# Optimization experiments

Hardware: AMD Instinct MI355X
Metric: run time of the kernel (lower is better)

## Reference

```python
import jax, jax.numpy as jnp
import numpy as np

H, IN, L, R = 128, 64, 3, 7
Nc, Na, Nx = 10000, 40000, 100000
NS = (Nc, Na, Nx)
ES = (50000, 100000, 100000, 150000, 200000, 200000, 200000)
# relation order: cc, c->a, a->c, aa, a->x, x->a, xx  (0=core,1=agg,2=access)
SRC_T = (0, 0, 1, 1, 1, 2, 2)
DST_T = (0, 1, 0, 1, 2, 1, 2)


def setup_inputs() -> dict:
    key = jax.random.key(0)
    ks = iter(jax.random.split(key, 80))
    d = {}
    for name, n in (("x_core", Nc), ("x_agg", Na), ("x_access", Nx)):
        d[name] = jax.random.normal(next(ks), (n, IN), jnp.float32)
    for r in range(R):
        d[f"src{r}"] = jax.random.randint(next(ks), (ES[r],), 0, NS[SRC_T[r]])
        d[f"dst{r}"] = jax.random.randint(next(ks), (ES[r],), 0, NS[DST_T[r]])
        d[f"ea{r}"] = jax.random.normal(next(ks), (ES[r], 3), jnp.float32)

    def w(k, shape, fan):
        return (jax.random.normal(k, shape, jnp.float32) / np.float32(np.sqrt(fan)))

    for nt in ("core", "agg", "access"):
        d[f"linW_{nt}"] = w(next(ks), (IN, H), IN)
        d[f"linb_{nt}"] = jnp.zeros((H,), jnp.float32)
    d["eW"] = w(next(ks), (L, R, 3, H), 3)       # GINEConv edge Linear(3->H)
    d["eb"] = jnp.zeros((L, R, H), jnp.float32)
    d["W1"] = w(next(ks), (L, R, H, H), H)        # MLP first Linear
    d["b1"] = jnp.zeros((L, R, H), jnp.float32)
    d["g1"] = jnp.ones((L, R, H), jnp.float32)    # BatchNorm gamma
    d["be1"] = jnp.zeros((L, R, H), jnp.float32)  # BatchNorm beta
    d["W2"] = w(next(ks), (L, R, H, H), H)        # MLP second Linear
    d["b2"] = jnp.zeros((L, R, H), jnp.float32)
    return d


def _forward(x_core, x_agg, x_access,
             linW_core, linb_core, linW_agg, linb_agg, linW_access, linb_access,
             eW, eb, W1, b1, g1, be1, W2, b2, srcs, dsts, eas):
    elu = jax.nn.elu
    h = [elu(x_core @ linW_core + linb_core),
         elu(x_agg @ linW_agg + linb_agg),
         elu(x_access @ linW_access + linb_access)]
    bn_inv = 1.0 / jnp.sqrt(jnp.float32(1.0 + 1e-5))  # eval BN: running mean 0, var 1
    for l in range(L):
        out = [jnp.zeros_like(ht) for ht in h]
        for r in range(R):
            s, t = SRC_T[r], DST_T[r]
            # GINEConv message: ReLU(x_j + Lin(edge_attr))  -> [E, H]
            msg = jax.nn.relu(h[s][srcs[r]] + eas[r] @ eW[l, r] + eb[l, r])
            agg = jax.ops.segment_sum(msg, dsts[r], num_segments=h[t].shape[0])
            z = h[t] + agg  # (1+eps)*x_i + aggr, eps=0
            # PyG MLP([H,H,H]): Linear -> BatchNorm -> ReLU -> Linear
            z = jax.nn.relu((z @ W1[l, r] + b1[l, r]) * bn_inv * g1[l, r] + be1[l, r])
            out[t] = out[t] + (z @ W2[l, r] + b2[l, r])  # HeteroConv aggr='sum'
        # residual + ELU; dropout is identity in eval mode
        h = [elu(out[t] + h[t]) for t in range(3)]
    return tuple(h)


def reference(x_core, x_agg, x_access,
              src0, dst0, ea0, src1, dst1, ea1, src2, dst2, ea2,
              src3, dst3, ea3, src4, dst4, ea4, src5, dst5, ea5,
              src6, dst6, ea6,
              linW_core, linb_core, linW_agg, linb_agg, linW_access, linb_access,
              eW, eb, W1, b1, g1, be1, W2, b2):
    srcs = (src0, src1, src2, src3, src4, src5, src6)
    dsts = (dst0, dst1, dst2, dst3, dst4, dst5, dst6)
    eas = (ea0, ea1, ea2, ea3, ea4, ea5, ea6)
    return _forward(x_core, x_agg, x_access,
                    linW_core, linb_core, linW_agg, linb_agg, linW_access, linb_access,
                    eW, eb, W1, b1, g1, be1, W2, b2, srcs, dsts, eas)
```

## Files before the change

kernel.cpp:

```cpp
#include <hip/hip_runtime.h>
#include <math.h>

#define H 128

typedef __attribute__((ext_vector_type(8))) short short8;
typedef __attribute__((ext_vector_type(4))) float f32x4;

static const int SRC_T_[7] = {0, 0, 1, 1, 1, 2, 2};
static const int DST_T_[7] = {0, 1, 0, 1, 2, 1, 2};

__device__ __forceinline__ float eluf(float x) {
    return x > 0.f ? x : (__expf(x) - 1.f);
}
__device__ __forceinline__ unsigned short f2bf(float x) {
    union { float f; unsigned int u; } v; v.f = x;
    unsigned int r = v.u + 0x7fffu + ((v.u >> 16) & 1u);
    return (unsigned short)(r >> 16);
}
__device__ __forceinline__ float bf2f(unsigned int u) {
    union { unsigned int u; float f; } v; v.u = u << 16;
    return v.f;
}

__global__ __launch_bounds__(128) void k_input_linear(
    const float* __restrict__ x, const float* __restrict__ W,
    const float* __restrict__ b, unsigned short* __restrict__ hb, int n)
{
    __shared__ float Ws[64 * H];
    __shared__ float xs[16 * 64];
    __shared__ unsigned short os[16 * H];
    const int j = threadIdx.x;
    for (int i = j; i < 64 * H; i += 128) Ws[i] = W[i];
    const float bj = b[j];

    for (int r0 = blockIdx.x * 16; r0 < n; r0 += gridDim.x * 16) {
        const int nrows = min(16, n - r0);
        __syncthreads();
        for (int i = j; i < nrows * 64; i += 128) xs[i] = x[(size_t)r0 * 64 + i];
        __syncthreads();
        for (int i = 0; i < nrows; ++i) {
            float acc = bj;
#pragma unroll
            for (int k = 0; k < 64; k += 4) {
                float4 xv = *(const float4*)&xs[i * 64 + k];
                acc += xv.x * Ws[(k + 0) * H + j] + xv.y * Ws[(k + 1) * H + j]
                     + xv.z * Ws[(k + 2) * H + j] + xv.w * Ws[(k + 3) * H + j];
            }
            os[i * H + j] = f2bf(eluf(acc));
        }
        __syncthreads();
        uint2* d = (uint2*)&hb[(size_t)r0 * H];
        const uint2* s2 = (const uint2*)os;
        for (int i = j; i < nrows * 32; i += 128) d[i] = s2[i];
    }
}

struct CsrCtx {
    const int* src[7]; const int* dst[7]; const float* ea[7];
    int* csr_src[7]; uint2* csr_ea[7]; int* ptr[7];
    int* deg; int* cursor; int* bsum;
    int eOff[8];
    int bOff[8];
    int nd[7];
};

__global__ __launch_bounds__(256) void k_hist_all(CsrCtx C, int Etot)
{
    for (int e = blockIdx.x * 256 + threadIdx.x; e < Etot; e += gridDim.x * 256) {
        int r = 0;
        while (e >= C.eOff[r + 1]) ++r;
        const int le = e - C.eOff[r];
        atomicAdd(&C.deg[(C.bOff[r] << 8) + C.dst[r][le]], 1);
    }
}

__global__ __launch_bounds__(256) void k_scan_partial_all(CsrCtx C)
{
    __shared__ int s[256];
    const int b = blockIdx.x;
    int r = 0;
    while (b >= C.bOff[r + 1]) ++r;
    const int lb = b - C.bOff[r];
    const int tid = threadIdx.x;
    const int idx = lb * 256 + tid;
    s[tid] = idx < C.nd[r] ? C.deg[(C.bOff[r] << 8) + idx] : 0;
    __syncthreads();
    for (int off = 128; off > 0; off >>= 1) {
        if (tid < off) s[tid] += s[tid + off];
        __syncthreads();
    }
    if (tid == 0) C.bsum[b] = s[0];
}

__global__ __launch_bounds__(512) void k_scan_mid_all(CsrCtx C)
{
    __shared__ int s[512];
    const int r = blockIdx.x;
    const int nb = C.bOff[r + 1] - C.bOff[r];
    const int tid = threadIdx.x;
    const int v = tid < nb ? C.bsum[C.bOff[r] + tid] : 0;
    s[tid] = v;
    __syncthreads();
    for (int off = 1; off < 512; off <<= 1) {
        int t = (tid >= off) ? s[tid - off] : 0;
        __syncthreads();
        s[tid] += t;
        __syncthreads();
    }
    if (tid < nb) C.bsum[C.bOff[r] + tid] = s[tid] - v;
    if (tid == nb - 1) C.ptr[r][C.nd[r]] = s[tid];
}

__global__ __launch_bounds__(256) void k_scan_final_all(CsrCtx C)
{
    __shared__ int s[256];
    const int b = blockIdx.x;
    int r = 0;
    while (b >= C.bOff[r + 1]) ++r;
    const int lb = b - C.bOff[r];
    const int tid = threadIdx.x;
    const int idx = lb * 256 + tid;
    const int v = idx < C.nd[r] ? C.deg[(C.bOff[r] << 8) + idx] : 0;
    s[tid] = v;
    __syncthreads();
    for (int off = 1; off < 256; off <<= 1) {
        int t = (tid >= off) ? s[tid - off] : 0;
        __syncthreads();
        s[tid] += t;
        __syncthreads();
    }
    if (idx < C.nd[r]) {
        const int excl = s[tid] - v + C.bsum[b];
        C.ptr[r][idx] = excl;
        C.cursor[(C.bOff[r] << 8) + idx] = excl;
    }
}

__global__ __launch_bounds__(256) void k_scatter_all(CsrCtx C, int Etot)
{
    for (int e = blockIdx.x * 256 + threadIdx.x; e < Etot; e += gridDim.x * 256) {
        int r = 0;
        while (e >= C.eOff[r + 1]) ++r;
        const int le = e - C.eOff[r];
        const int d = C.dst[r][le];
        const int pos = atomicAdd(&C.cursor[(C.bOff[r] << 8) + d], 1);
        C.csr_src[r][pos] = C.src[r][le];
        const float* eap = C.ea[r] + (size_t)3 * le;
        uint2 p;
        p.x = (unsigned int)f2bf(eap[0]) | ((unsigned int)f2bf(eap[1]) << 16);
        p.y = (unsigned int)f2bf(eap[2]);
        C.csr_ea[r][pos] = p;
    }
}

__global__ __launch_bounds__(256) void k_wprep(
    const float* __restrict__ W1, const float* __restrict__ W2,
    unsigned short* __restrict__ wp, int total)
{
    for (int i = blockIdx.x * 256 + threadIdx.x; i < total; i += gridDim.x * 256) {
        int lr = i >> 14, rem = i & 16383;
        int c = rem >> 7, k = rem & 127;
        wp[(size_t)(lr * 2 + 0) * 16384 + rem] = f2bf(W1[(size_t)lr * 16384 + k * H + c]);
        wp[(size_t)(lr * 2 + 1) * 16384 + rem] = f2bf(W2[(size_t)lr * 16384 + k * H + c]);
    }
}

struct AggCtx {
    const int* ptr[7]; const int* csr_src[7]; const uint2* csr_ea[7];
    const unsigned short* hsrc[7]; const unsigned short* hdst[7];
    unsigned short* z[7];
    int gOff[8];
    int nd[7];
};

__global__ __launch_bounds__(256) void k_aggz_all(
    AggCtx A, const float* __restrict__ eW, const float* __restrict__ eb, int l)
{
    const int b = blockIdx.x;
    int r = 0;
    while (b >= A.gOff[r + 1]) ++r;
    const int lb = b - A.gOff[r];
    const int wave = threadIdx.x >> 6;
    const int lane = threadIdx.x & 63;
    const int t2 = lane << 1;
    const int lr = l * 7 + r;
    const float* eWr = eW + (size_t)lr * 3 * H;
    const float* ebr = eb + (size_t)lr * H;
    const float w00 = eWr[t2],         w01 = eWr[t2 + 1];
    const float w10 = eWr[H + t2],     w11 = eWr[H + t2 + 1];
    const float w20 = eWr[2 * H + t2], w21 = eWr[2 * H + t2 + 1];
    const float b0 = ebr[t2], b1v = ebr[t2 + 1];

    const int nd = A.nd[r];
    const int d0 = lb * 64 + wave * 16;
    if (d0 >= nd) return;
    const int dend = min(d0 + 16, nd);
    const int* __restrict__ ptr = A.ptr[r];
    const int* __restrict__ cs = A.csr_src[r];
    const uint2* __restrict__ ce = A.csr_ea[r];
    const unsigned short* __restrict__ hs = A.hsrc[r];
    const unsigned short* __restrict__ hd = A.hdst[r];
    unsigned int* __restrict__ zp = (unsigned int*)A.z[r];

    int p1 = ptr[d0];
    for (int d = d0; d < dend; ++d) {
        const int p0 = p1;
        p1 = ptr[d + 1];
        const unsigned int hdv = ((const unsigned int*)&hd[(size_t)d * H])[lane];
        float acc0 = bf2f(hdv & 0xffffu);
        float acc1 = bf2f(hdv >> 16);
        int i = p0;
        for (; i + 1 < p1; i += 2) {
            const int s0 = cs[i], s1 = cs[i + 1];
            const uint2 e0 = ce[i], e1 = ce[i + 1];
            const unsigned int hv0 = ((const unsigned int*)&hs[(size_t)s0 * H])[lane];
            const unsigned int hv1 = ((const unsigned int*)&hs[(size_t)s1 * H])[lane];
            const float a00 = bf2f(e0.x & 0xffffu), a01 = bf2f(e0.x >> 16), a02 = bf2f(e0.y & 0xffffu);
            const float a10 = bf2f(e1.x & 0xffffu), a11 = bf2f(e1.x >> 16), a12 = bf2f(e1.y & 0xffffu);
            acc0 += fmaxf(bf2f(hv0 & 0xffffu) + a00 * w00 + a01 * w10 + a02 * w20 + b0, 0.f)
                  + fmaxf(bf2f(hv1 & 0xffffu) + a10 * w00 + a11 * w10 + a12 * w20 + b0, 0.f);
            acc1 += fmaxf(bf2f(hv0 >> 16) + a00 * w01 + a01 * w11 + a02 * w21 + b1v, 0.f)
                  + fmaxf(bf2f(hv1 >> 16) + a10 * w01 + a11 * w11 + a12 * w21 + b1v, 0.f);
        }
        if (i < p1) {
            const int s = cs[i];
            const uint2 ep = ce[i];
            const float a0 = bf2f(ep.x & 0xffffu);
            const float a1 = bf2f(ep.x >> 16);
            const float a2 = bf2f(ep.y & 0xffffu);
            const unsigned int hv = ((const unsigned int*)&hs[(size_t)s * H])[lane];
            acc0 += fmaxf(bf2f(hv & 0xffffu) + a0 * w00 + a1 * w10 + a2 * w20 + b0, 0.f);
            acc1 += fmaxf(bf2f(hv >> 16)     + a0 * w01 + a1 * w11 + a2 * w21 + b1v, 0.f);
        }
        zp[(size_t)d * 64 + lane] =
            (unsigned int)f2bf(acc0) | ((unsigned int)f2bf(acc1) << 16);
    }
}

struct MlpCtx {
    const unsigned short* z[3][3];
    int lr[3][3];
    int nrel[3];
    int gend[3];
    int noffH[3];
    int n[3];
};

__global__ __launch_bounds__(512, 4) void k_mlp_all(
    MlpCtx M, const unsigned short* __restrict__ hb,
    unsigned short* __restrict__ hbw, float* __restrict__ fout,
    const unsigned short* __restrict__ wprep,
    const float* __restrict__ b1g, const float* __restrict__ g1g,
    const float* __restrict__ be1g, const float* __restrict__ b2g, int fin)
{
    __shared__ unsigned short zt[128 * H];
    __shared__ unsigned short a1t[128 * H];

    const int b = blockIdx.x;
    const int t = (b >= M.gend[0] ? 1 : 0) + (b >= M.gend[1] ? 1 : 0);
    const int lb = b - (t == 0 ? 0 : M.gend[t - 1]);
    const int n = M.n[t];
    const int nrel = M.nrel[t];
    const unsigned short* hbp = hb + (size_t)M.noffH[t];

    const int tid = threadIdx.x;
    const int lane = tid & 63;
    const int wave = tid >> 6;
    const int wr = wave >> 2;
    const int wc = wave & 3;
    const int l15 = lane & 15;
    const int lq  = lane >> 4;
    const int c0 = wc * 32 + l15;

    const int r0 = lb * 128;
    const int rows = min(128, n - r0);

    const float bn_inv = 0.99999500003749977f;
    const f32x4 Z4 = {0.f, 0.f, 0.f, 0.f};
    f32x4 acc2[4][2];
#pragma unroll
    for (int rb = 0; rb < 4; ++rb)
#pragma unroll
        for (int nf = 0; nf < 2; ++nf) acc2[rb][nf] = Z4;
    float b2s0 = 0.f, b2s1 = 0.f;

    for (int rl = 0; rl < nrel; ++rl) {
        const unsigned short* z = M.z[t][rl];
        const int lr = M.lr[t][rl];
        const unsigned short* wp = wprep + (size_t)lr * 32768;
        const float b1c0 = b1g[lr * H + c0],            b1c1 = b1g[lr * H + c0 + 16];
        const float sc0  = g1g[lr * H + c0] * bn_inv,   sc1  = g1g[lr * H + c0 + 16] * bn_inv;
        const float be0  = be1g[lr * H + c0],           be1v = be1g[lr * H + c0 + 16];
        b2s0 += b2g[lr * H + c0]; b2s1 += b2g[lr * H + c0 + 16];

        if (rows == 128) {
            uint4 v[4];
#pragma unroll
            for (int it = 0; it < 4; ++it) {
                const int idx = tid + it * 512;
                const int row = idx >> 4, cg = (idx & 15) << 3;
                v[it] = *(const uint4*)&z[(size_t)(r0 + row) * H + cg];
            }
#pragma unroll
            for (int it = 0; it < 4; ++it) {
                const int idx = tid + it * 512;
                const int row = idx >> 4, cg = (idx & 15) << 3;
                *(uint4*)&zt[row * H + (cg ^ ((row & 7) << 3))] = v[it];
            }
        } else {
            for (int idx = tid; idx < rows * 16; idx += 512) {
                const int row = idx >> 4, cg = (idx & 15) << 3;
                uint4 v = *(const uint4*)&z[(size_t)(r0 + row) * H + cg];
                *(uint4*)&zt[row * H + (cg ^ ((row & 7) << 3))] = v;
            }
        }
        __syncthreads();

        f32x4 acc1[4][2];
#pragma unroll
        for (int rb = 0; rb < 4; ++rb)
#pragma unroll
            for (int nf = 0; nf < 2; ++nf) acc1[rb][nf] = Z4;
#pragma unroll
        for (int kc = 0; kc < 4; ++kc) {
            const int kb = kc * 32 + (lq << 3);
            short8 af[4], wf[2];
#pragma unroll
            for (int rb = 0; rb < 4; ++rb) {
                const int row = wr * 64 + rb * 16 + l15;
                af[rb] = *(const short8*)&zt[row * H + (kb ^ ((row & 7) << 3))];
            }
#pragma unroll
            for (int nf = 0; nf < 2; ++nf)
                wf[nf] = *(const short8*)&wp[(c0 + nf * 16) * H + kb];
#pragma unroll
            for (int rb = 0; rb < 4; ++rb)
#pragma unroll
                for (int nf = 0; nf < 2; ++nf)
                    acc1[rb][nf] = __builtin_amdgcn_mfma_f32_16x16x32_bf16(
                        af[rb], wf[nf], acc1[rb][nf], 0, 0, 0);
        }
#pragma unroll
        for (int rb = 0; rb < 4; ++rb)
#pragma unroll
            for (int nf = 0; nf < 2; ++nf) {
                const int col = c0 + nf * 16;
                const float b1c = nf == 0 ? b1c0 : b1c1;
                const float scv = nf == 0 ? sc0 : sc1;
                const float bev = nf == 0 ? be0 : be1v;
#pragma unroll
                for (int rg = 0; rg < 4; ++rg) {
                    const int row = wr * 64 + rb * 16 + (lq << 2) + rg;
                    float v = fmaxf((acc1[rb][nf][rg] + b1c) * scv + bev, 0.f);
                    a1t[row * H + (col ^ ((row & 7) << 3))] = f2bf(v);
                }
            }
        __syncthreads();

#pragma unroll
        for (int kc = 0; kc < 4; ++kc) {
            const int kb = kc * 32 + (lq << 3);
            short8 af[4], wf[2];
#pragma unroll
            for (int rb = 0; rb < 4; ++rb) {
                const int row = wr * 64 + rb * 16 + l15;
                af[rb] = *(const short8*)&a1t[row * H + (kb ^ ((row & 7) << 3))];
            }
#pragma unroll
            for (int nf = 0; nf < 2; ++nf)
                wf[nf] = *(const short8*)&wp[16384 + (c0 + nf * 16) * H + kb];
#pragma unroll
            for (int rb = 0; rb < 4; ++rb)
#pragma unroll
                for (int nf = 0; nf < 2; ++nf)
                    acc2[rb][nf] = __builtin_amdgcn_mfma_f32_16x16x32_bf16(
                        af[rb], wf[nf], acc2[rb][nf], 0, 0, 0);
        }
    }

    if (fin) {
        float* foutp = fout + (size_t)M.noffH[t];
#pragma unroll
        for (int rb = 0; rb < 4; ++rb)
#pragma unroll
            for (int nf = 0; nf < 2; ++nf) {
                const int col = c0 + nf * 16;
                const float b2s = nf == 0 ? b2s0 : b2s1;
#pragma unroll
                for (int rg = 0; rg < 4; ++rg) {
                    const int row = wr * 64 + rb * 16 + (lq << 2) + rg;
                    if (row < rows) {
                        const size_t o = (size_t)(r0 + row) * H + col;
                        foutp[o] = eluf(acc2[rb][nf][rg] + b2s
                                        + bf2f((unsigned int)hbp[o]));
                    }
                }
            }
    } else {
        unsigned short* hbwp = hbw + (size_t)M.noffH[t];
        __syncthreads();
#pragma unroll
        for (int rb = 0; rb < 4; ++rb)
#pragma unroll
            for (int nf = 0; nf < 2; ++nf) {
                const int col = c0 + nf * 16;
                const float b2s = nf == 0 ? b2s0 : b2s1;
#pragma unroll
                for (int rg = 0; rg < 4; ++rg) {
                    const int row = wr * 64 + rb * 16 + (lq << 2) + rg;
                    if (row < rows) {
                        const size_t o = (size_t)(r0 + row) * H + col;
                        a1t[row * H + col] = f2bf(eluf(acc2[rb][nf][rg] + b2s
                                                       + bf2f((unsigned int)hbp[o])));
                    }
                }
            }
        __syncthreads();
        uint2* d = (uint2*)&hbwp[(size_t)r0 * H];
        const uint2* s2 = (const uint2*)a1t;
        for (int idx = tid; idx < rows * 32; idx += 512) d[idx] = s2[idx];
    }
}

static inline int imin(int a, int b) { return a < b ? a : b; }
static inline size_t alignup(size_t x) { return (x + 255) & ~(size_t)255; }

extern "C" void kernel_launch(void* const* d_in, const int* in_sizes, int n_in,
                              void* d_out, int out_size, void* d_ws, size_t ws_size,
                              hipStream_t stream) {
    const float* xin[3] = {(const float*)d_in[0], (const float*)d_in[1], (const float*)d_in[2]};
    const int* src[7]; const int* dst[7]; const float* ea[7]; int E[7];
    for (int r = 0; r < 7; ++r) {
        src[r] = (const int*)d_in[3 + 3 * r];
        dst[r] = (const int*)d_in[4 + 3 * r];
        ea[r]  = (const float*)d_in[5 + 3 * r];
        E[r]   = in_sizes[3 + 3 * r];
    }
    const float* linW[3] = {(const float*)d_in[24], (const float*)d_in[26], (const float*)d_in[28]};
    const float* linb[3] = {(const float*)d_in[25], (const float*)d_in[27], (const float*)d_in[29]};
    const float* eW  = (const float*)d_in[30];
    const float* ebp = (const float*)d_in[31];
    const float* W1  = (const float*)d_in[32];
    const float* b1  = (const float*)d_in[33];
    const float* g1  = (const float*)d_in[34];
    const float* be1 = (const float*)d_in[35];
    const float* W2  = (const float*)d_in[36];
    const float* b2  = (const float*)d_in[37];

    const int NSn[3]  = {in_sizes[0] / 64, in_sizes[1] / 64, in_sizes[2] / 64};
    const int NTOT = NSn[0] + NSn[1] + NSn[2];
    const int noff[3] = {0, NSn[0], NSn[0] + NSn[1]};

    float* fout = (float*)d_out;

    int eOff[8]; eOff[0] = 0;
    for (int r = 0; r < 7; ++r) eOff[r + 1] = eOff[r] + E[r];
    const int Etot = eOff[7];
    int bOff[8]; bOff[0] = 0;
    for (int r = 0; r < 7; ++r) bOff[r + 1] = bOff[r] + (NSn[DST_T_[r]] + 255) / 256;
    int gOff[8]; gOff[0] = 0;
    for (int r = 0; r < 7; ++r) gOff[r + 1] = gOff[r] + (NSn[DST_T_[r]] + 63) / 64;

    char* wsb = (char*)d_ws;
    size_t off = 0;
    unsigned short* hb = (unsigned short*)(wsb + off); off = alignup(off + (size_t)NTOT * H * 2);
    unsigned short* zb[7];
    for (int r = 0; r < 7; ++r) {
        int nd = NSn[DST_T_[r]];
        zb[r] = (unsigned short*)(wsb + off); off = alignup(off + (size_t)nd * H * 2);
    }
    unsigned short* wprep = (unsigned short*)(wsb + off); off = alignup(off + (size_t)21 * 32768 * 2);
    int* deg    = (int*)(wsb + off); off = alignup(off + (size_t)bOff[7] * 256 * 4);
    int* cursor = (int*)(wsb + off); off = alignup(off + (size_t)bOff[7] * 256 * 4);
    int* bsum   = (int*)(wsb + off); off = alignup(off + (size_t)bOff[7] * 4 + 256);
    int* ptrs[7]; int* csrs[7]; uint2* ceas[7];
    for (int r = 0; r < 7; ++r) {
        int nd = NSn[DST_T_[r]];
        ptrs[r] = (int*)(wsb + off); off = alignup(off + (size_t)(nd + 1) * 4);
    }
    for (int r = 0; r < 7; ++r) {
        csrs[r] = (int*)(wsb + off); off = alignup(off + (size_t)E[r] * 4);
    }
    for (int r = 0; r < 7; ++r) {
        ceas[r] = (uint2*)(wsb + off); off = alignup(off + (size_t)E[r] * 8);
    }

    CsrCtx C;
    for (int r = 0; r < 7; ++r) {
        C.src[r] = src[r]; C.dst[r] = dst[r]; C.ea[r] = ea[r];
        C.csr_src[r] = csrs[r]; C.csr_ea[r] = ceas[r]; C.ptr[r] = ptrs[r];
        C.nd[r] = NSn[DST_T_[r]];
    }
    C.deg = deg; C.cursor = cursor; C.bsum = bsum;
    for (int r = 0; r < 8; ++r) { C.eOff[r] = eOff[r]; C.bOff[r] = bOff[r]; }

    hipMemsetAsync(deg, 0, (size_t)bOff[7] * 256 * 4, stream);
    k_hist_all<<<imin((Etot + 255) / 256, 8192), 256, 0, stream>>>(C, Etot);
    k_scan_partial_all<<<bOff[7], 256, 0, stream>>>(C);
    k_scan_mid_all<<<7, 512, 0, stream>>>(C);
    k_scan_final_all<<<bOff[7], 256, 0, stream>>>(C);
    k_scatter_all<<<imin((Etot + 255) / 256, 8192), 256, 0, stream>>>(C, Etot);
    k_wprep<<<1344, 256, 0, stream>>>(W1, W2, wprep, 21 * 16384);

    for (int t = 0; t < 3; ++t) {
        int n = NSn[t];
        k_input_linear<<<imin((n + 15) / 16, 2048), 128, 0, stream>>>(
            xin[t], linW[t], linb[t], hb + (size_t)noff[t] * H, n);
    }

    AggCtx A;
    for (int r = 0; r < 7; ++r) {
        A.ptr[r] = ptrs[r]; A.csr_src[r] = csrs[r]; A.csr_ea[r] = ceas[r];
        A.hsrc[r] = hb + (size_t)noff[SRC_T_[r]] * H;
        A.hdst[r] = hb + (size_t)noff[DST_T_[r]] * H;
        A.z[r] = zb[r];
        A.nd[r] = NSn[DST_T_[r]];
    }
    for (int r = 0; r < 8; ++r) A.gOff[r] = gOff[r];

    static const int RELS[3][3] = {{0, 2, 0}, {1, 3, 5}, {4, 6, 0}};
    static const int NRELS[3] = {2, 3, 2};
    MlpCtx M;
    int gend = 0;
    for (int t = 0; t < 3; ++t) {
        M.nrel[t] = NRELS[t];
        M.noffH[t] = noff[t] * H;
        M.n[t] = NSn[t];
        gend += (NSn[t] + 127) / 128;
        M.gend[t] = gend;
        for (int k = 0; k < 3; ++k) M.z[t][k] = zb[RELS[t][k]];
    }

    for (int l = 0; l < 3; ++l) {
        const int fin = (l == 2) ? 1 : 0;
        k_aggz_all<<<gOff[7], 256, 0, stream>>>(A, eW, ebp, l);
        for (int t = 0; t < 3; ++t)
            for (int k = 0; k < 3; ++k) M.lr[t][k] = l * 7 + RELS[t][k];
        k_mlp_all<<<M.gend[2], 512, 0, stream>>>(
            M, hb, hb, fout, wprep, b1, g1, be1, b2, fin);
    }
}
```

Before: 913.2 us.

## Prefetch next relation's z tile via direct global-to-LDS loads with pre-swizzled layout

The aggregation kernel now writes z rows with an XOR swizzle already applied, so the MLP kernel can copy tiles into LDS verbatim using global_load_lds instead of staging through registers. The copy of the next relation's tile is issued right after the first GEMM finishes reading zt, so it overlaps with the second GEMM. W1 fragments are also hoisted into registers once per relation. This adds register pressure and depends on correct sync between the async LDS writes and later reads.

```diff
diff --git a/kernel.cpp b/kernel.cpp
--- a/kernel.cpp
+++ b/kernel.cpp
@@ -21,6 +21,10 @@
     union { unsigned int u; float f; } v; v.u = u << 16;
     return v.f;
 }
+
+#define GLDS16(gp, lp) __builtin_amdgcn_global_load_lds( \
+    (const __attribute__((address_space(1))) void*)(gp), \
+    (__attribute__((address_space(3))) void*)(lp), 16, 0, 0)
 
 __global__ __launch_bounds__(128) void k_input_linear(
     const float* __restrict__ x, const float* __restrict__ W,
@@ -232,7 +236,7 @@
             acc0 += fmaxf(bf2f(hv & 0xffffu) + a0 * w00 + a1 * w10 + a2 * w20 + b0, 0.f);
             acc1 += fmaxf(bf2f(hv >> 16)     + a0 * w01 + a1 * w11 + a2 * w21 + b1v, 0.f);
         }
-        zp[(size_t)d * 64 + lane] =
+        zp[(size_t)d * 64 + (lane ^ ((d & 7) << 2))] =
             (unsigned int)f2bf(acc0) | ((unsigned int)f2bf(acc1) << 16);
     }
 }
@@ -274,6 +278,22 @@
 
     const int r0 = lb * 128;
     const int rows = min(128, n - r0);
+    const bool full = (rows == 128);
+
+    auto stage = [&](const unsigned short* z) {
+        const unsigned short* zsrc = z + (size_t)r0 * H;
+        if (full) {
+#pragma unroll
+            for (int it = 0; it < 4; ++it) {
+                const int off = (wave * 4 + it) * 512;
+                GLDS16(zsrc + off + lane * 8, zt + off);
+            }
+        } else {
+            for (int idx = tid; idx < rows * 16; idx += 512) {
+                *(uint4*)&zt[idx * 8] = *(const uint4*)&zsrc[idx * 8];
+            }
+        }
+    };
 
     const float bn_inv = 0.99999500003749977f;
     const f32x4 Z4 = {0.f, 0.f, 0.f, 0.f};
@@ -284,36 +304,22 @@
         for (int nf = 0; nf < 2; ++nf) acc2[rb][nf] = Z4;
     float b2s0 = 0.f, b2s1 = 0.f;
 
+    stage(M.z[t][0]);
+
     for (int rl = 0; rl < nrel; ++rl) {
-        const unsigned short* z = M.z[t][rl];
         const int lr = M.lr[t][rl];
         const unsigned short* wp = wprep + (size_t)lr * 32768;
+        short8 w1f[2][4];
+#pragma unroll
+        for (int nf = 0; nf < 2; ++nf)
+#pragma unroll
+            for (int kc = 0; kc < 4; ++kc)
+                w1f[nf][kc] = *(const short8*)&wp[(c0 + nf * 16) * H + kc * 32 + (lq << 3)];
         const float b1c0 = b1g[lr * H + c0],            b1c1 = b1g[lr * H + c0 + 16];
         const float sc0  = g1g[lr * H + c0] * bn_inv,   sc1  = g1g[lr * H + c0 + 16] * bn_inv;
         const float be0  = be1g[lr * H + c0],           be1v = be1g[lr * H + c0 + 16];
         b2s0 += b2g[lr * H + c0]; b2s1 += b2g[lr * H + c0 + 16];
 
-        if (rows == 128) {
-            uint4 v[4];
-#pragma unroll
-            for (int it = 0; it < 4; ++it) {
-                const int idx = tid + it * 512;
-                const int row = idx >> 4, cg = (idx & 15) << 3;
-                v[it] = *(const uint4*)&z[(size_t)(r0 + row) * H + cg];
-            }
-#pragma unroll
-            for (int it = 0; it < 4; ++it) {
-                const int idx = tid + it * 512;
-                const int row = idx >> 4, cg = (idx & 15) << 3;
-                *(uint4*)&zt[row * H + (cg ^ ((row & 7) << 3))] = v[it];
-            }
-        } else {
-            for (int idx = tid; idx < rows * 16; idx += 512) {
-                const int row = idx >> 4, cg = (idx & 15) << 3;
-                uint4 v = *(const uint4*)&z[(size_t)(r0 + row) * H + cg];
-                *(uint4*)&zt[row * H + (cg ^ ((row & 7) << 3))] = v;
-            }
-        }
         __syncthreads();
 
         f32x4 acc1[4][2];
@@ -324,21 +330,18 @@
 #pragma unroll
         for (int kc = 0; kc < 4; ++kc) {
             const int kb = kc * 32 + (lq << 3);
-            short8 af[4], wf[2];
+            short8 af[4];
 #pragma unroll
             for (int rb = 0; rb < 4; ++rb) {
                 const int row = wr * 64 + rb * 16 + l15;
                 af[rb] = *(const short8*)&zt[row * H + (kb ^ ((row & 7) << 3))];
             }
 #pragma unroll
-            for (int nf = 0; nf < 2; ++nf)
-                wf[nf] = *(const short8*)&wp[(c0 + nf * 16) * H + kb];
-#pragma unroll
             for (int rb = 0; rb < 4; ++rb)
 #pragma unroll
                 for (int nf = 0; nf < 2; ++nf)
                     acc1[rb][nf] = __builtin_amdgcn_mfma_f32_16x16x32_bf16(
-                        af[rb], wf[nf], acc1[rb][nf], 0, 0, 0);
+                        af[rb], w1f[nf][kc], acc1[rb][nf], 0, 0, 0);
         }
 #pragma unroll
         for (int rb = 0; rb < 4; ++rb)
@@ -356,6 +359,8 @@
                 }
             }
         __syncthreads();
+
+        if (rl + 1 < nrel) stage(M.z[t][rl + 1]);
 
 #pragma unroll
         for (int kc = 0; kc < 4; ++kc) {
```

Measured after the change: 896.3 us. About the same (-1.8%).
